# Kernel optimization log

Hardware: AMD Instinct MI355X
Metric: run time of the kernel (lower is better)

Reference implementation:

```python
import jax, jax.numpy as jnp
import numpy as np
from jax import lax

SCALES = [2 ** i for i in range(9)]  # h_grid_global(9, 2**8): dyadic scales 1..256
EPS = 2e-5


def conv1d(x, w, dil, pad):
    # x: [B, Cin, X], w: [Cout, Cin, k]; 'same'-style padding pad on each side, rhs dilation dil
    return lax.conv_general_dilated(x, w, window_strides=(1,), padding=[(pad, pad)],
                                    rhs_dilation=(dil,), dimension_numbers=('NCH', 'OIH', 'NCH'))


def maxpool2_x(x):
    # max pool kernel=2 stride=2 over last (spatial) axis, floor mode like torch
    L = x.shape[-1]
    L2 = (L // 2) * 2
    x = x[..., :L2]
    return jnp.max(x.reshape(x.shape[:-1] + (L2 // 2, 2)), axis=-1)


def lift_conv(x, w):
    k = w.shape[-1]
    outs = [conv1d(x, w, s, s * (k // 2)) / s for s in SCALES]
    return jnp.stack(outs, axis=2)


def gg_conv(x, w):
    # GConvGG with h_crop: x [B, Cin, H, X], w [Cout, Cin, nh=3, k] -> [B, Cout, H-2, X]
    # output scale index i uses input scale slabs i..i+2, x-dilation = scale_i, 1/scale_i normalization
    B, Cin, H, X = x.shape
    Cout, _, nh, k = w.shape
    wf = w.reshape(Cout, Cin * nh, k)
    outs = []
    for i in range(H - nh + 1):
        xi = x[:, :, i:i + nh, :].reshape(B, Cin * nh, X)
        s = SCALES[i]
        outs.append(conv1d(xi, wf, s, s * (k // 2)) / s)
    return jnp.stack(outs, axis=2)


def batchnorm(x, g, b):
    # BatchNorm2d (training batch stats, biased var) over [B, C, H, X]
    m = jnp.mean(x, axis=(0, 2, 3), keepdims=True)
    v = jnp.mean((x - m) ** 2, axis=(0, 2, 3), keepdims=True)
    gb = g[None, :, None, None]
    bb = b[None, :, None, None]
    return gb * (x - m) * lax.rsqrt(v + EPS) + bb


def _winit(key, shape):
    fan = int(np.prod(shape[1:]))
    return jax.random.normal(key, shape, dtype=jnp.float32) * (fan ** -0.5)


def setup_inputs() -> dict:
    key = jax.random.key(0)
    ks = jax.random.split(key, 12)
    B = 4096
    nc = 12
    x = jax.random.normal(ks[0], (B, 100, 6), dtype=jnp.float32)
    inp = {
        'x': x,
        'w1': _winit(ks[1], (nc, 6, 7)),
        'w2': _winit(ks[2], (nc * 2, nc, 3, 5)),
        'w3': _winit(ks[3], (nc * 4, nc * 2, 3, 5)),
        'w4': _winit(ks[4], (nc * 8, nc * 4, 3, 3)),
        'g1': jnp.ones((nc,), jnp.float32), 'b1': jnp.zeros((nc,), jnp.float32),
        'g2': jnp.ones((nc * 2,), jnp.float32), 'b2': jnp.zeros((nc * 2,), jnp.float32),
        'g3': jnp.ones((nc * 4,), jnp.float32), 'b3': jnp.zeros((nc * 4,), jnp.float32),
        'g4': jnp.ones((nc * 8,), jnp.float32), 'b4': jnp.zeros((nc * 8,), jnp.float32),
        'f1w': _winit(ks[5], (nc * 8, nc * 8 * 3)), 'f1b': jnp.zeros((nc * 8,), jnp.float32),
        'f2w': _winit(ks[6], (nc * 4, nc * 8)), 'f2b': jnp.zeros((nc * 4,), jnp.float32),
        'f3w': _winit(ks[7], (6, nc * 4)), 'f3b': jnp.zeros((6,), jnp.float32),
    }
    return inp


def reference(x, w1, w2, w3, w4, g1, b1, g2, b2, g3, b3, g4, b4,
              f1w, f1b, f2w, f2b, f3w, f3b):
    h = jnp.transpose(x, (0, 2, 1))          # [B, 6, 100]
    h = lift_conv(h, w1)                     # [B, 12, 9, 100]
    h = maxpool2_x(h)                        # [B, 12, 9, 50]
    h = batchnorm(jax.nn.relu(h), g1, b1)
    h = maxpool2_x(h)                        # [B, 12, 9, 25]
    h = gg_conv(h, w2)                       # [B, 24, 7, 25]
    h = maxpool2_x(h)                        # [B, 24, 7, 12]
    h = batchnorm(jax.nn.relu(h), g2, b2)
    h = maxpool2_x(h)                        # [B, 24, 7, 6]
    h = gg_conv(h, w3)                       # [B, 48, 5, 6]
    h = maxpool2_x(h)                        # [B, 48, 5, 3]
    h = batchnorm(jax.nn.relu(h), g3, b3)
    h = gg_conv(h, w4)                       # [B, 96, 3, 3]
    h = maxpool2_x(h)                        # [B, 96, 3, 1]
    h = batchnorm(jax.nn.relu(h), g4, b4)
    h = h.reshape(h.shape[0], -1)            # [B, 288]
    h = h @ f1w.T + f1b                      # dropout is identity in eval
    h = h @ f2w.T + f2b
    return h @ f3w.T + f3b                   # [B, 6]
```

## Files before the change

### kernel.cpp

```cpp
#include <hip/hip_runtime.h>
#include <hip/hip_fp16.h>

#define EPSBN 2e-5f

typedef _Float16 hf2 __attribute__((ext_vector_type(2)));

static __device__ __forceinline__ float fdot2h(hf2 a, hf2 b, float c) {
  return __builtin_amdgcn_fdot2(a, b, c, false);
}
static __device__ __forceinline__ unsigned pk(float a, float b) {
  union { __half2 h; unsigned u; } u;
  u.h = __floats2half2_rn(a, b);
  return u.u;
}

__global__ __launch_bounds__(256) void k_prep(const float* __restrict__ w1,
    const float* __restrict__ w2, const float* __restrict__ w3, const float* __restrict__ w4,
    __half* __restrict__ W1P, __half* __restrict__ W2P,
    __half* __restrict__ W3P, __half* __restrict__ W4P) {
  int i = blockIdx.x * 256 + threadIdx.x;
  if (i < 504) {
    int ci = i & 1, r = i >> 1, o = r % 12, j = (r / 12) % 7, cp = r / 84, c = 2 * cp + ci;
    W1P[i] = __float2half_rn(w1[(o * 6 + c) * 7 + j]);
  }
  if (i < 4320) {
    int ci = i & 1, r = i >> 1, o = r % 24, j = (r / 24) % 5, h = (r / 120) % 3, cp = r / 360;
    int c = 2 * cp + ci;
    W2P[i] = __float2half_rn(w2[((o * 12 + c) * 3 + h) * 5 + j]);
  }
  if (i < 17280) {
    int ci = i & 1, r = i >> 1, o = r % 48, j = (r / 48) % 5, h = (r / 240) % 3, cp = r / 720;
    int c = 2 * cp + ci;
    W3P[i] = __float2half_rn(w3[((o * 24 + c) * 3 + h) * 5 + j]);
  }
  if (i < 41472) {
    int ci = i & 1, r = i >> 1, o48 = r % 48, j = (r / 48) % 3, h = (r / 144) % 3;
    int cp = (r / 432) % 24, ch = r / 10368, c = 2 * cp + ci, o = ch * 48 + o48;
    W4P[i] = __float2half_rn(w4[((o * 48 + c) * 3 + h) * 3 + j]);
  }
}

#define NB1 4
template<int SI>
__device__ __forceinline__ void s1_si(const unsigned* __restrict__ xsu, int bb, int t0,
    const unsigned* __restrict__ wlu, int o0, bool act, int b,
    __half* __restrict__ r1, float& ts0, float& tq0, float& ts1, float& tq1) {
  constexpr int S = 1 << SI;
  float a0[10], a1[10];
#pragma unroll
  for (int k = 0; k < 10; ++k) { a0[k] = 0.f; a1[k] = 0.f; }
#pragma unroll 1
  for (int cp = 0; cp < 3; ++cp) {
    const hf2* xr = (const hf2*)xsu + (bb * 3 + cp) * 295 + 96 + t0;
    const unsigned* wp = wlu + cp * 84;
#pragma unroll
    for (int j = 0; j < 7; ++j) {
      const int off = S * (j - 3);
      if (off < -96 || off > 98) continue;
      hf2 w0 = *(const hf2*)(wp + j * 12 + o0);
      hf2 w1 = *(const hf2*)(wp + j * 12 + o0 + 1);
      hf2 xv[10];
#pragma unroll
      for (int k = 0; k < 10; ++k) xv[k] = xr[off + k];
#pragma unroll
      for (int k = 0; k < 10; ++k) {
        a0[k] = fdot2h(xv[k], w0, a0[k]);
        a1[k] = fdot2h(xv[k], w1, a1[k]);
      }
    }
  }
  if (act) {
    const float inv = 1.0f / (float)S;
    size_t rb = ((size_t)b * 12 + o0) * 9 + SI;
#pragma unroll
    for (int u = 0; u < 5; ++u) {
      float v0 = fmaxf(fmaxf(a0[2 * u], a0[2 * u + 1]) * inv, 0.f);
      float v1 = fmaxf(fmaxf(a1[2 * u], a1[2 * u + 1]) * inv, 0.f);
      r1[rb * 50 + (t0 >> 1) + u] = __float2half_rn(v0);
      r1[(rb + 9) * 50 + (t0 >> 1) + u] = __float2half_rn(v1);
      ts0 += v0; tq0 += v0 * v0; ts1 += v1; tq1 += v1 * v1;
    }
  }
}

__global__ __launch_bounds__(256) void k_lift(const float* __restrict__ x,
    const __half* __restrict__ W1P, __half* __restrict__ r1,
    float* __restrict__ sum, float* __restrict__ sq) {
  __shared__ unsigned xsu[NB1 * 885];
  __shared__ unsigned wlu[252];
  __shared__ float ssum[12], ssq[12];
  int b0 = blockIdx.x * NB1, tid = threadIdx.x;
  for (int i = tid; i < NB1 * 885; i += 256) xsu[i] = 0u;
  for (int i = tid; i < 252; i += 256) wlu[i] = ((const unsigned*)W1P)[i];
  if (tid < 12) { ssum[tid] = 0.f; ssq[tid] = 0.f; }
  __syncthreads();
  __half* xsh = (__half*)xsu;
  for (int i = tid; i < NB1 * 600; i += 256) {
    int bb = i / 600, f = i % 600, t = f / 6, c = f % 6;
    xsh[((bb * 3 + (c >> 1)) * 295 + 96 + t) * 2 + (c & 1)] =
        __float2half_rn(x[(size_t)(b0 + bb) * 600 + f]);
  }
  __syncthreads();
  bool act = tid < 240;
  int task = act ? tid : 0;
  int bb = task / 60, r = task % 60;
  int op = r / 10, tc = r % 10;
  int o0 = op * 2, t0 = tc * 10;
  int b = b0 + bb;
  float ts0 = 0.f, tq0 = 0.f, ts1 = 0.f, tq1 = 0.f;
  s1_si<0>(xsu, bb, t0, wlu, o0, act, b, r1, ts0, tq0, ts1, tq1);
  s1_si<1>(xsu, bb, t0, wlu, o0, act, b, r1, ts0, tq0, ts1, tq1);
  s1_si<2>(xsu, bb, t0, wlu, o0, act, b, r1, ts0, tq0, ts1, tq1);
  s1_si<3>(xsu, bb, t0, wlu, o0, act, b, r1, ts0, tq0, ts1, tq1);
  s1_si<4>(xsu, bb, t0, wlu, o0, act, b, r1, ts0, tq0, ts1, tq1);
  s1_si<5>(xsu, bb, t0, wlu, o0, act, b, r1, ts0, tq0, ts1, tq1);
  s1_si<6>(xsu, bb, t0, wlu, o0, act, b, r1, ts0, tq0, ts1, tq1);
  s1_si<7>(xsu, bb, t0, wlu, o0, act, b, r1, ts0, tq0, ts1, tq1);
  s1_si<8>(xsu, bb, t0, wlu, o0, act, b, r1, ts0, tq0, ts1, tq1);
  if (act) {
    atomicAdd(&ssum[o0], ts0); atomicAdd(&ssq[o0], tq0);
    atomicAdd(&ssum[o0 + 1], ts1); atomicAdd(&ssq[o0 + 1], tq1);
  }
  __syncthreads();
  if (tid < 12) { atomicAdd(&sum[tid], ssum[tid]); atomicAdd(&sq[tid], ssq[tid]); }
}

__global__ void k_bnstat(const float* __restrict__ sum, const float* __restrict__ sq,
    const float* __restrict__ g, const float* __restrict__ bb,
    float* __restrict__ sc, float* __restrict__ sh, int C, float invN) {
  int c = threadIdx.x;
  if (c < C) {
    float m = sum[c] * invN;
    float v = sq[c] * invN - m * m;
    float scale = g[c] * rsqrtf(v + EPSBN);
    sc[c] = scale;
    sh[c] = bb[c] - m * scale;
  }
}

#define NB2 5
template<int S, int I2>
__device__ __forceinline__ void s2_do(const unsigned* __restrict__ abu,
    const unsigned* __restrict__ wlu, int op, bool act, int b,
    __half* __restrict__ r2p, float& ts0, float& tq0, float& ts1, float& tq1) {
  float acc0[24], acc1[24];
#pragma unroll
  for (int t = 0; t < 24; ++t) { acc0[t] = 0.f; acc1[t] = 0.f; }
#pragma unroll 1
  for (int cp = 0; cp < 6; ++cp) {
#pragma unroll
    for (int h = 0; h < 3; ++h) {
      const hf2* ar = (const hf2*)(abu + (cp * 9 + I2 + h) * 26);
      hf2 rr[25];
#pragma unroll
      for (int t = 0; t < 25; ++t) rr[t] = ar[t];
      const unsigned* wp = wlu + ((cp * 3 + h) * 5) * 24 + op * 2;
#pragma unroll
      for (int j = 0; j < 5; ++j) {
        const int off = S * (j - 2);
        if (off <= -25 || off >= 25) continue;
        hf2 w0 = *(const hf2*)(wp + j * 24);
        hf2 w1 = *(const hf2*)(wp + j * 24 + 1);
#pragma unroll
        for (int t = 0; t < 24; ++t) {
          if (t + off >= 0 && t + off < 25) {
            acc0[t] = fdot2h(rr[t + off], w0, acc0[t]);
            acc1[t] = fdot2h(rr[t + off], w1, acc1[t]);
          }
        }
      }
    }
  }
  if (act) {
    const float inv = 1.0f / (float)S;
    int o0 = op * 2;
    __half* p0 = r2p + ((size_t)b * 24 + o0) * 42 + I2 * 6;
    __half* p1 = p0 + 42;
    float m0 = 0.f, m1 = 0.f;
#pragma unroll
    for (int u = 0; u < 12; ++u) {
      float v0 = fmaxf(fmaxf(acc0[2 * u], acc0[2 * u + 1]) * inv, 0.f);
      float v1 = fmaxf(fmaxf(acc1[2 * u], acc1[2 * u + 1]) * inv, 0.f);
      ts0 += v0; tq0 += v0 * v0; ts1 += v1; tq1 += v1 * v1;
      if ((u & 1) == 0) { m0 = v0; m1 = v1; }
      else {
        p0[u >> 1] = __float2half_rn(fmaxf(m0, v0));
        p1[u >> 1] = __float2half_rn(fmaxf(m1, v1));
      }
    }
  }
}

__global__ __launch_bounds__(256) void k_stage2(const __half* __restrict__ r1,
    const __half* __restrict__ W2P, const float* __restrict__ sc, const float* __restrict__ sh,
    __half* __restrict__ r2p, float* __restrict__ sum, float* __restrict__ sq, int B) {
  __shared__ unsigned asu[NB2 * 1405];
  __shared__ unsigned wlu[2160];
  __shared__ float ssum[24], ssq[24];
  int b0 = blockIdx.x * NB2, tid = threadIdx.x;
  for (int i = tid; i < NB2 * 1350; i += 256) {
    int bb = i / 1350, s = i % 1350;
    if (b0 + bb < B) {
      int cp = s / 225, rem = s % 225, row = rem / 25, t = rem % 25;
      int c0 = 2 * cp, c1 = c0 + 1;
      float2 a0 = __half22float2(*(const __half2*)(r1 +
          (((size_t)(b0 + bb) * 12 + c0) * 9 + row) * 50 + 2 * t));
      float2 a1 = __half22float2(*(const __half2*)(r1 +
          (((size_t)(b0 + bb) * 12 + c1) * 9 + row) * 50 + 2 * t));
      float v0 = fmaxf(a0.x, a0.y) * sc[c0] + sh[c0];
      float v1 = fmaxf(a1.x, a1.y) * sc[c1] + sh[c1];
      asu[bb * 1405 + (cp * 9 + row) * 26 + t] = pk(v0, v1);
    }
  }
  for (int i = tid; i < 540; i += 256)
    ((uint4*)wlu)[i] = ((const uint4*)W2P)[i];
  if (tid < 24) { ssum[tid] = 0.f; ssq[tid] = 0.f; }
  __syncthreads();
  int wv = tid >> 6, lane = tid & 63;
  int bb = lane / 12, op = lane % 12;
  bool act = (lane < 60) && (b0 + bb < B);
  if (bb > 4) bb = 4;
  const unsigned* abu = asu + bb * 1405;
  int b = b0 + bb;
  float ts0 = 0.f, tq0 = 0.f, ts1 = 0.f, tq1 = 0.f;
  if (wv == 0) {
    s2_do<1, 0>(abu, wlu, op, act, b, r2p, ts0, tq0, ts1, tq1);
  } else if (wv == 1) {
    s2_do<2, 1>(abu, wlu, op, act, b, r2p, ts0, tq0, ts1, tq1);
    s2_do<64, 6>(abu, wlu, op, act, b, r2p, ts0, tq0, ts1, tq1);
  } else if (wv == 2) {
    s2_do<4, 2>(abu, wlu, op, act, b, r2p, ts0, tq0, ts1, tq1);
    s2_do<32, 5>(abu, wlu, op, act, b, r2p, ts0, tq0, ts1, tq1);
  } else {
    s2_do<8, 3>(abu, wlu, op, act, b, r2p, ts0, tq0, ts1, tq1);
    s2_do<16, 4>(abu, wlu, op, act, b, r2p, ts0, tq0, ts1, tq1);
  }
  if (act) {
    int o0 = op * 2;
    atomicAdd(&ssum[o0], ts0); atomicAdd(&ssq[o0], tq0);
    atomicAdd(&ssum[o0 + 1], ts1); atomicAdd(&ssq[o0 + 1], tq1);
  }
  __syncthreads();
  if (tid < 24) { atomicAdd(&sum[tid], ssum[tid]); atomicAdd(&sq[tid], ssq[tid]); }
}

#define NB3 8
template<int I2>
__device__ __forceinline__ void s3h(const hf2* __restrict__ rr, int h,
    const hf2* __restrict__ w0, const hf2* __restrict__ w1, float* __restrict__ acc) {
  constexpr int S = 1 << I2;
  const int base = (I2 + h) * 6;
#pragma unroll
  for (int j = 0; j < 5; ++j) {
    const int off = S * (j - 2);
    if (off <= -6 || off >= 6) continue;
#pragma unroll
    for (int t = 0; t < 6; ++t) {
      if (t + off >= 0 && t + off < 6) {
        acc[t] = fdot2h(rr[base + t + off], w0[j], acc[t]);
        acc[6 + t] = fdot2h(rr[base + t + off], w1[j], acc[6 + t]);
      }
    }
  }
}

__global__ __launch_bounds__(256) void k_stage3(const __half* __restrict__ r2p,
    const __half* __restrict__ W3P, const float* __restrict__ sc, const float* __restrict__ sh,
    __half* __restrict__ r3, float* __restrict__ sum, float* __restrict__ sq) {
  __shared__ unsigned asu[NB3 * 505];
  __shared__ unsigned wlu[8640];
  __shared__ float ssum[48], ssq[48];
  int b0 = blockIdx.x * NB3, tid = threadIdx.x;
  for (int i = tid; i < NB3 * 252; i += 256) {
    int bb = i / 252, s = i % 252;
    int cp = s / 21, rem = s % 21, row = rem / 3, tp = rem % 3;
    int c0 = 2 * cp, c1 = c0 + 1;
    float2 a0 = __half22float2(*(const __half2*)(r2p +
        (((size_t)(b0 + bb) * 24 + c0) * 7 + row) * 6 + 2 * tp));
    float2 a1 = __half22float2(*(const __half2*)(r2p +
        (((size_t)(b0 + bb) * 24 + c1) * 7 + row) * 6 + 2 * tp));
    float v00 = a0.x * sc[c0] + sh[c0], v01 = a0.y * sc[c0] + sh[c0];
    float v10 = a1.x * sc[c1] + sh[c1], v11 = a1.y * sc[c1] + sh[c1];
    int di = bb * 505 + (cp * 7 + row) * 6 + 2 * tp;
    asu[di] = pk(v00, v10);
    asu[di + 1] = pk(v01, v11);
  }
  for (int i = tid; i < 2160; i += 256)
    ((uint4*)wlu)[i] = ((const uint4*)W3P)[i];
  if (tid < 48) { ssum[tid] = 0.f; ssq[tid] = 0.f; }
  __syncthreads();
  bool act = tid < 192;
  int bb = act ? tid / 24 : 0, op = tid % 24;
  int b = b0 + bb;
  if (act) {
    float acc[60];
#pragma unroll
    for (int k = 0; k < 60; ++k) acc[k] = 0.f;
#pragma unroll 1
    for (int cp = 0; cp < 12; ++cp) {
      const hf2* ar = (const hf2*)(asu + bb * 505 + cp * 42);
      hf2 rr[42];
#pragma unroll
      for (int k = 0; k < 42; ++k) rr[k] = ar[k];
#pragma unroll
      for (int h = 0; h < 3; ++h) {
        const unsigned* wp = wlu + (cp * 15 + h * 5) * 48 + op * 2;
        hf2 w0[5], w1[5];
#pragma unroll
        for (int j = 0; j < 5; ++j) {
          w0[j] = *(const hf2*)(wp + j * 48);
          w1[j] = *(const hf2*)(wp + j * 48 + 1);
        }
        s3h<0>(rr, h, w0, w1, acc);
        s3h<1>(rr, h, w0, w1, acc + 12);
        s3h<2>(rr, h, w0, w1, acc + 24);
        s3h<3>(rr, h, w0, w1, acc + 36);
        s3h<4>(rr, h, w0, w1, acc + 48);
      }
    }
    float ts0 = 0.f, tq0 = 0.f, ts1 = 0.f, tq1 = 0.f;
    int ob = op * 2;
#pragma unroll
    for (int i2 = 0; i2 < 5; ++i2) {
      const float inv = 1.0f / (float)(1 << i2);
      size_t rb0 = ((size_t)b * 48 + ob) * 15 + i2 * 3;
#pragma unroll
      for (int u = 0; u < 3; ++u) {
        float v0 = fmaxf(fmaxf(acc[i2 * 12 + 2 * u], acc[i2 * 12 + 2 * u + 1]) * inv, 0.f);
        float v1 = fmaxf(fmaxf(acc[i2 * 12 + 6 + 2 * u], acc[i2 * 12 + 7 + 2 * u]) * inv, 0.f);
        r3[rb0 + u] = __float2half_rn(v0);
        r3[rb0 + 15 + u] = __float2half_rn(v1);
        ts0 += v0; tq0 += v0 * v0; ts1 += v1; tq1 += v1 * v1;
      }
    }
    atomicAdd(&ssum[ob], ts0); atomicAdd(&ssq[ob], tq0);
    atomicAdd(&ssum[ob + 1], ts1); atomicAdd(&ssq[ob + 1], tq1);
  }
  __syncthreads();
  if (tid < 48) { atomicAdd(&sum[tid], ssum[tid]); atomicAdd(&sq[tid], ssq[tid]); }
}

#define NB4 8
template<int I2>
__device__ __forceinline__ void s4h(const hf2* __restrict__ rr, int h,
    const hf2* __restrict__ w0, const hf2* __restrict__ w1, float* __restrict__ acc) {
  constexpr int S = 1 << I2;
  const int base = (I2 + h) * 3;
#pragma unroll
  for (int j = 0; j < 3; ++j) {
    const int off = S * (j - 1);
    if (off <= -3 || off >= 3) continue;
    if (off >= 0) {
      acc[0] = fdot2h(rr[base + off], w0[j], acc[0]);
      acc[2] = fdot2h(rr[base + off], w1[j], acc[2]);
    }
    const int i1 = 1 + off;
    if (i1 >= 0 && i1 < 3) {
      acc[1] = fdot2h(rr[base + i1], w0[j], acc[1]);
      acc[3] = fdot2h(rr[base + i1], w1[j], acc[3]);
    }
  }
}

__global__ __launch_bounds__(256) void k_stage4(const __half* __restrict__ r3,
    const __half* __restrict__ W4P, const float* __restrict__ sc, const float* __restrict__ sh,
    float* __restrict__ r4, float* __restrict__ sum, float* __restrict__ sq) {
  __shared__ unsigned asu[NB4 * 361];
  __shared__ unsigned wlu[10368];
  __shared__ float ssum[96], ssq[96];
  int b0 = blockIdx.x * NB4, tid = threadIdx.x;
  for (int i = tid; i < NB4 * 360; i += 256) {
    int bb = i / 360, s = i % 360;
    int cp = s / 15, rem = s % 15, row = rem / 3, t = rem % 3;
    int c0 = 2 * cp, c1 = c0 + 1;
    float v0 = __half2float(r3[(((size_t)(b0 + bb) * 48 + c0) * 5 + row) * 3 + t]) * sc[c0] + sh[c0];
    float v1 = __half2float(r3[(((size_t)(b0 + bb) * 48 + c1) * 5 + row) * 3 + t]) * sc[c1] + sh[c1];
    asu[bb * 361 + (cp * 5 + row) * 3 + t] = pk(v0, v1);
  }
  if (tid < 96) { ssum[tid] = 0.f; ssq[tid] = 0.f; }
  bool act = tid < 192;
  int bb = act ? tid / 24 : 0, op = tid % 24;
  int b = b0 + bb;
  for (int chunk = 0; chunk < 2; ++chunk) {
    __syncthreads();
    for (int i = tid; i < 2592; i += 256)
      ((uint4*)wlu)[i] = ((const uint4*)W4P)[chunk * 2592 + i];
    __syncthreads();
    if (act) {
      float acc[12];
#pragma unroll
      for (int k = 0; k < 12; ++k) acc[k] = 0.f;
#pragma unroll 1
      for (int cp = 0; cp < 24; ++cp) {
        const hf2* ar = (const hf2*)(asu + bb * 361 + cp * 15);
        hf2 rr[15];
#pragma unroll
        for (int k = 0; k < 15; ++k) rr[k] = ar[k];
#pragma unroll
        for (int h = 0; h < 3; ++h) {
          const unsigned* wp = wlu + ((cp * 3 + h) * 3) * 48 + op * 2;
          hf2 w0[3], w1[3];
#pragma unroll
          for (int j = 0; j < 3; ++j) {
            w0[j] = *(const hf2*)(wp + j * 48);
            w1[j] = *(const hf2*)(wp + j * 48 + 1);
          }
          s4h<0>(rr, h, w0, w1, acc);
          s4h<1>(rr, h, w0, w1, acc + 4);
          s4h<2>(rr, h, w0, w1, acc + 8);
        }
      }
      int o0 = chunk * 48 + op * 2;
#pragma unroll
      for (int oo = 0; oo < 2; ++oo) {
        float ts = 0.f, tq = 0.f;
#pragma unroll
        for (int i2 = 0; i2 < 3; ++i2) {
          const float inv = 1.0f / (float)(1 << i2);
          float v = fmaxf(fmaxf(acc[i2 * 4 + oo * 2], acc[i2 * 4 + oo * 2 + 1]) * inv, 0.f);
          r4[(size_t)b * 288 + (o0 + oo) * 3 + i2] = v;
          ts += v; tq += v * v;
        }
        atomicAdd(&ssum[o0 + oo], ts); atomicAdd(&ssq[o0 + oo], tq);
      }
    }
  }
  __syncthreads();
  if (tid < 96) { atomicAdd(&sum[tid], ssum[tid]); atomicAdd(&sq[tid], ssq[tid]); }
}

__global__ __launch_bounds__(256) void k_fc(const float* __restrict__ r4,
    const float* __restrict__ sc, const float* __restrict__ sh,
    const float* __restrict__ f1w, const float* __restrict__ f1b,
    const float* __restrict__ f2w, const float* __restrict__ f2b,
    const float* __restrict__ f3w, const float* __restrict__ f3b,
    float* __restrict__ out) {
  __shared__ float v[4][288];
  __shared__ float h1[4][96];
  __shared__ float h2[4][48];
  int b0 = blockIdx.x * 4, tid = threadIdx.x;
  for (int i = tid; i < 4 * 288; i += 256) {
    int bb = i / 288, f = i % 288, c = f / 3;
    v[bb][f] = r4[(size_t)(b0 + bb) * 288 + f] * sc[c] + sh[c];
  }
  __syncthreads();
  for (int d = tid; d < 384; d += 256) {
    int o = d >> 2, bb = d & 3;
    const float* wr = &f1w[o * 288];
    const float* vv = v[bb];
    float acc = f1b[o];
    for (int f = 0; f < 288; ++f) acc += wr[f] * vv[f];
    h1[bb][o] = acc;
  }
  __syncthreads();
  if (tid < 192) {
    int o = tid >> 2, bb = tid & 3;
    const float* wr = &f2w[o * 96];
    float acc = f2b[o];
    for (int f = 0; f < 96; ++f) acc += wr[f] * h1[bb][f];
    h2[bb][o] = acc;
  }
  __syncthreads();
  if (tid < 24) {
    int o = tid >> 2, bb = tid & 3;
    const float* wr = &f3w[o * 48];
    float acc = f3b[o];
    for (int f = 0; f < 48; ++f) acc += wr[f] * h2[bb][f];
    out[(size_t)(b0 + bb) * 6 + o] = acc;
  }
}

extern "C" void kernel_launch(void* const* d_in, const int* in_sizes, int n_in,
                              void* d_out, int out_size, void* d_ws, size_t ws_size,
                              hipStream_t stream) {
  const float* x   = (const float*)d_in[0];
  const float* w1  = (const float*)d_in[1];
  const float* w2  = (const float*)d_in[2];
  const float* w3  = (const float*)d_in[3];
  const float* w4  = (const float*)d_in[4];
  const float* g1  = (const float*)d_in[5];
  const float* b1  = (const float*)d_in[6];
  const float* g2  = (const float*)d_in[7];
  const float* b2  = (const float*)d_in[8];
  const float* g3  = (const float*)d_in[9];
  const float* b3  = (const float*)d_in[10];
  const float* g4  = (const float*)d_in[11];
  const float* b4  = (const float*)d_in[12];
  const float* f1w = (const float*)d_in[13];
  const float* f1b = (const float*)d_in[14];
  const float* f2w = (const float*)d_in[15];
  const float* f2b = (const float*)d_in[16];
  const float* f3w = (const float*)d_in[17];
  const float* f3b = (const float*)d_in[18];
  float* out = (float*)d_out;
  float* ws = (float*)d_ws;

  const int B = 4096;
  float* SUM1 = ws + 0;   float* SQ1 = ws + 12;
  float* SUM2 = ws + 24;  float* SQ2 = ws + 48;
  float* SUM3 = ws + 72;  float* SQ3 = ws + 120;
  float* SUM4 = ws + 168; float* SQ4 = ws + 264;
  float* SC1 = ws + 384;  float* SH1 = ws + 396;
  float* SC2 = ws + 408;  float* SH2 = ws + 432;
  float* SC3 = ws + 456;  float* SH3 = ws + 504;
  float* SC4 = ws + 552;  float* SH4 = ws + 648;
  __half* H0  = (__half*)(ws + 1024);
  __half* W1P = H0;
  __half* W2P = H0 + 512;
  __half* W3P = H0 + 4864;
  __half* W4P = H0 + 22272;
  __half* R1h = H0 + 65536;
  __half* R2p = R1h + (size_t)B * 5400;
  __half* R3h = R1h;
  float*  R4  = (float*)(R2p + (size_t)B * 1008);

  hipMemsetAsync(d_ws, 0, 384 * sizeof(float), stream);

  k_prep<<<162, 256, 0, stream>>>(w1, w2, w3, w4, W1P, W2P, W3P, W4P);
  k_lift<<<B / NB1, 256, 0, stream>>>(x, W1P, R1h, SUM1, SQ1);
  k_bnstat<<<1, 128, 0, stream>>>(SUM1, SQ1, g1, b1, SC1, SH1, 12, 1.0f / (float)(B * 450));
  k_stage2<<<(B + NB2 - 1) / NB2, 256, 0, stream>>>(R1h, W2P, SC1, SH1, R2p, SUM2, SQ2, B);
  k_bnstat<<<1, 128, 0, stream>>>(SUM2, SQ2, g2, b2, SC2, SH2, 24, 1.0f / (float)(B * 84));
  k_stage3<<<B / NB3, 256, 0, stream>>>(R2p, W3P, SC2, SH2, R3h, SUM3, SQ3);
  k_bnstat<<<1, 128, 0, stream>>>(SUM3, SQ3, g3, b3, SC3, SH3, 48, 1.0f / (float)(B * 15));
  k_stage4<<<B / NB4, 256, 0, stream>>>(R3h, W4P, SC3, SH3, R4, SUM4, SQ4);
  k_bnstat<<<1, 128, 0, stream>>>(SUM4, SQ4, g4, b4, SC4, SH4, 96, 1.0f / (float)(B * 3));
  k_fc<<<B / 4, 256, 0, stream>>>(R4, SC4, SH4, f1w, f1b, f2w, f2b, f3w, f3b, out);
}
```

Before: 321.3 us.

## Fold weight prep and BN stat kernels into stage kernels; pack intermediates as half2

Removes the separate weight-packing kernel by doing the weight conversion inside k_lift, and removes the four single-block BN-statistics kernels by computing scale and shift in each consumer kernel's prologue. Intermediates r2 and r3 are now stored channel-pair-interleaved as packed half2 words, so the next stage loads one 32-bit word per pair and no longer gathers two scattered halves. This cuts five launches and some strided traffic, at the cost of redundant per-block BN math and extra work in the first blocks of k_lift.

```diff
diff --git a/kernel.cpp b/kernel.cpp
--- a/kernel.cpp
+++ b/kernel.cpp
@@ -13,31 +13,9 @@
   u.h = __floats2half2_rn(a, b);
   return u.u;
 }
-
-__global__ __launch_bounds__(256) void k_prep(const float* __restrict__ w1,
-    const float* __restrict__ w2, const float* __restrict__ w3, const float* __restrict__ w4,
-    __half* __restrict__ W1P, __half* __restrict__ W2P,
-    __half* __restrict__ W3P, __half* __restrict__ W4P) {
-  int i = blockIdx.x * 256 + threadIdx.x;
-  if (i < 504) {
-    int ci = i & 1, r = i >> 1, o = r % 12, j = (r / 12) % 7, cp = r / 84, c = 2 * cp + ci;
-    W1P[i] = __float2half_rn(w1[(o * 6 + c) * 7 + j]);
-  }
-  if (i < 4320) {
-    int ci = i & 1, r = i >> 1, o = r % 24, j = (r / 24) % 5, h = (r / 120) % 3, cp = r / 360;
-    int c = 2 * cp + ci;
-    W2P[i] = __float2half_rn(w2[((o * 12 + c) * 3 + h) * 5 + j]);
-  }
-  if (i < 17280) {
-    int ci = i & 1, r = i >> 1, o = r % 48, j = (r / 48) % 5, h = (r / 240) % 3, cp = r / 720;
-    int c = 2 * cp + ci;
-    W3P[i] = __float2half_rn(w3[((o * 24 + c) * 3 + h) * 5 + j]);
-  }
-  if (i < 41472) {
-    int ci = i & 1, r = i >> 1, o48 = r % 48, j = (r / 48) % 3, h = (r / 144) % 3;
-    int cp = (r / 432) % 24, ch = r / 10368, c = 2 * cp + ci, o = ch * 48 + o48;
-    W4P[i] = __float2half_rn(w4[((o * 48 + c) * 3 + h) * 3 + j]);
-  }
+static __device__ __forceinline__ float2 uph(unsigned v) {
+  union { unsigned u; __half2 h; } x; x.u = v;
+  return __half22float2(x.h);
 }
 
 #define NB1 4
@@ -84,14 +62,37 @@
 }
 
 __global__ __launch_bounds__(256) void k_lift(const float* __restrict__ x,
-    const __half* __restrict__ W1P, __half* __restrict__ r1,
-    float* __restrict__ sum, float* __restrict__ sq) {
-  __shared__ unsigned xsu[NB1 * 885];
-  __shared__ unsigned wlu[252];
+    const float* __restrict__ w1, const float* __restrict__ w2,
+    const float* __restrict__ w3, const float* __restrict__ w4,
+    __half* __restrict__ W2P, __half* __restrict__ W3P, __half* __restrict__ W4P,
+    __half* __restrict__ r1, float* __restrict__ sum, float* __restrict__ sq) {
+  __shared__ __align__(16) unsigned xsu[NB1 * 885];
+  __shared__ __align__(16) unsigned wlu[252];
   __shared__ float ssum[12], ssq[12];
   int b0 = blockIdx.x * NB1, tid = threadIdx.x;
+  {
+    int gi = blockIdx.x * 256 + tid;
+    if (gi < 4320) {
+      int ci = gi & 1, r = gi >> 1, o = r % 24, j = (r / 24) % 5, h = (r / 120) % 3, cp = r / 360;
+      int c = 2 * cp + ci;
+      W2P[gi] = __float2half_rn(w2[((o * 12 + c) * 3 + h) * 5 + j]);
+    } else if (gi < 21600) {
+      int k = gi - 4320;
+      int ci = k & 1, r = k >> 1, o = r % 48, j = (r / 48) % 5, h = (r / 240) % 3, cp = r / 720;
+      int c = 2 * cp + ci;
+      W3P[k] = __float2half_rn(w3[((o * 24 + c) * 3 + h) * 5 + j]);
+    } else if (gi < 63072) {
+      int k = gi - 21600;
+      int ci = k & 1, r = k >> 1, o48 = r % 48, j = (r / 48) % 3, h = (r / 144) % 3;
+      int cp = (r / 432) % 24, ch = r / 10368, c = 2 * cp + ci, o = ch * 48 + o48;
+      W4P[k] = __float2half_rn(w4[((o * 48 + c) * 3 + h) * 3 + j]);
+    }
+  }
   for (int i = tid; i < NB1 * 885; i += 256) xsu[i] = 0u;
-  for (int i = tid; i < 252; i += 256) wlu[i] = ((const unsigned*)W1P)[i];
+  for (int i = tid; i < 252; i += 256) {
+    int cp = i / 84, j = (i % 84) / 12, o = i % 12;
+    wlu[i] = pk(w1[(o * 6 + 2 * cp) * 7 + j], w1[(o * 6 + 2 * cp + 1) * 7 + j]);
+  }
   if (tid < 12) { ssum[tid] = 0.f; ssq[tid] = 0.f; }
   __syncthreads();
   __half* xsh = (__half*)xsu;
@@ -125,24 +126,11 @@
   if (tid < 12) { atomicAdd(&sum[tid], ssum[tid]); atomicAdd(&sq[tid], ssq[tid]); }
 }
 
-__global__ void k_bnstat(const float* __restrict__ sum, const float* __restrict__ sq,
-    const float* __restrict__ g, const float* __restrict__ bb,
-    float* __restrict__ sc, float* __restrict__ sh, int C, float invN) {
-  int c = threadIdx.x;
-  if (c < C) {
-    float m = sum[c] * invN;
-    float v = sq[c] * invN - m * m;
-    float scale = g[c] * rsqrtf(v + EPSBN);
-    sc[c] = scale;
-    sh[c] = bb[c] - m * scale;
-  }
-}
-
 #define NB2 5
 template<int S, int I2>
 __device__ __forceinline__ void s2_do(const unsigned* __restrict__ abu,
     const unsigned* __restrict__ wlu, int op, bool act, int b,
-    __half* __restrict__ r2p, float& ts0, float& tq0, float& ts1, float& tq1) {
+    unsigned* __restrict__ r2p, float& ts0, float& tq0, float& ts1, float& tq1) {
   float acc0[24], acc1[24];
 #pragma unroll
   for (int t = 0; t < 24; ++t) { acc0[t] = 0.f; acc1[t] = 0.f; }
@@ -173,9 +161,7 @@
   }
   if (act) {
     const float inv = 1.0f / (float)S;
-    int o0 = op * 2;
-    __half* p0 = r2p + ((size_t)b * 24 + o0) * 42 + I2 * 6;
-    __half* p1 = p0 + 42;
+    unsigned* pd = r2p + ((size_t)b * 12 + op) * 42 + I2 * 6;
     float m0 = 0.f, m1 = 0.f;
 #pragma unroll
     for (int u = 0; u < 12; ++u) {
@@ -183,21 +169,30 @@
       float v1 = fmaxf(fmaxf(acc1[2 * u], acc1[2 * u + 1]) * inv, 0.f);
       ts0 += v0; tq0 += v0 * v0; ts1 += v1; tq1 += v1 * v1;
       if ((u & 1) == 0) { m0 = v0; m1 = v1; }
-      else {
-        p0[u >> 1] = __float2half_rn(fmaxf(m0, v0));
-        p1[u >> 1] = __float2half_rn(fmaxf(m1, v1));
-      }
+      else pd[u >> 1] = pk(fmaxf(m0, v0), fmaxf(m1, v1));
     }
   }
 }
 
 __global__ __launch_bounds__(256) void k_stage2(const __half* __restrict__ r1,
-    const __half* __restrict__ W2P, const float* __restrict__ sc, const float* __restrict__ sh,
-    __half* __restrict__ r2p, float* __restrict__ sum, float* __restrict__ sq, int B) {
-  __shared__ unsigned asu[NB2 * 1405];
-  __shared__ unsigned wlu[2160];
+    const __half* __restrict__ W2P,
+    const float* __restrict__ SUM, const float* __restrict__ SQ,
+    const float* __restrict__ g, const float* __restrict__ bbn, float invN,
+    unsigned* __restrict__ r2p, float* __restrict__ sum, float* __restrict__ sq, int B) {
+  __shared__ __align__(16) unsigned asu[NB2 * 1405];
+  __shared__ __align__(16) unsigned wlu[2160];
   __shared__ float ssum[24], ssq[24];
+  __shared__ float scf[12], shf[12];
   int b0 = blockIdx.x * NB2, tid = threadIdx.x;
+  if (tid < 12) {
+    float m = SUM[tid] * invN;
+    float v = SQ[tid] * invN - m * m;
+    float scale = g[tid] * rsqrtf(v + EPSBN);
+    scf[tid] = scale; shf[tid] = bbn[tid] - m * scale;
+    ssum[tid] = 0.f; ssq[tid] = 0.f;
+    ssum[tid + 12] = 0.f; ssq[tid + 12] = 0.f;
+  }
+  __syncthreads();
   for (int i = tid; i < NB2 * 1350; i += 256) {
     int bb = i / 1350, s = i % 1350;
     if (b0 + bb < B) {
@@ -207,14 +202,13 @@
           (((size_t)(b0 + bb) * 12 + c0) * 9 + row) * 50 + 2 * t));
       float2 a1 = __half22float2(*(const __half2*)(r1 +
           (((size_t)(b0 + bb) * 12 + c1) * 9 + row) * 50 + 2 * t));
-      float v0 = fmaxf(a0.x, a0.y) * sc[c0] + sh[c0];
-      float v1 = fmaxf(a1.x, a1.y) * sc[c1] + sh[c1];
+      float v0 = fmaxf(a0.x, a0.y) * scf[c0] + shf[c0];
+      float v1 = fmaxf(a1.x, a1.y) * scf[c1] + shf[c1];
       asu[bb * 1405 + (cp * 9 + row) * 26 + t] = pk(v0, v1);
     }
   }
   for (int i = tid; i < 540; i += 256)
     ((uint4*)wlu)[i] = ((const uint4*)W2P)[i];
-  if (tid < 24) { ssum[tid] = 0.f; ssq[tid] = 0.f; }
   __syncthreads();
   int wv = tid >> 6, lane = tid & 63;
   int bb = lane / 12, op = lane % 12;
@@ -264,30 +258,32 @@
   }
 }
 
-__global__ __launch_bounds__(256) void k_stage3(const __half* __restrict__ r2p,
-    const __half* __restrict__ W3P, const float* __restrict__ sc, const float* __restrict__ sh,
-    __half* __restrict__ r3, float* __restrict__ sum, float* __restrict__ sq) {
-  __shared__ unsigned asu[NB3 * 505];
-  __shared__ unsigned wlu[8640];
+__global__ __launch_bounds__(256) void k_stage3(const unsigned* __restrict__ r2p,
+    const __half* __restrict__ W3P,
+    const float* __restrict__ SUM, const float* __restrict__ SQ,
+    const float* __restrict__ g, const float* __restrict__ bbn, float invN,
+    unsigned* __restrict__ r3, float* __restrict__ sum, float* __restrict__ sq) {
+  __shared__ __align__(16) unsigned asu[NB3 * 505];
+  __shared__ __align__(16) unsigned wlu[8640];
   __shared__ float ssum[48], ssq[48];
+  __shared__ float scf[24], shf[24];
   int b0 = blockIdx.x * NB3, tid = threadIdx.x;
-  for (int i = tid; i < NB3 * 252; i += 256) {
-    int bb = i / 252, s = i % 252;
-    int cp = s / 21, rem = s % 21, row = rem / 3, tp = rem % 3;
+  if (tid < 24) {
+    float m = SUM[tid] * invN;
+    float v = SQ[tid] * invN - m * m;
+    float scale = g[tid] * rsqrtf(v + EPSBN);
+    scf[tid] = scale; shf[tid] = bbn[tid] - m * scale;
+  }
+  if (tid < 48) { ssum[tid] = 0.f; ssq[tid] = 0.f; }
+  __syncthreads();
+  for (int i = tid; i < NB3 * 504; i += 256) {
+    int bb = i / 504, f = i % 504, cp = f / 42;
     int c0 = 2 * cp, c1 = c0 + 1;
-    float2 a0 = __half22float2(*(const __half2*)(r2p +
-        (((size_t)(b0 + bb) * 24 + c0) * 7 + row) * 6 + 2 * tp));
-    float2 a1 = __half22float2(*(const __half2*)(r2p +
-        (((size_t)(b0 + bb) * 24 + c1) * 7 + row) * 6 + 2 * tp));
-    float v00 = a0.x * sc[c0] + sh[c0], v01 = a0.y * sc[c0] + sh[c0];
-    float v10 = a1.x * sc[c1] + sh[c1], v11 = a1.y * sc[c1] + sh[c1];
-    int di = bb * 505 + (cp * 7 + row) * 6 + 2 * tp;
-    asu[di] = pk(v00, v10);
-    asu[di + 1] = pk(v01, v11);
+    float2 a = uph(r2p[(size_t)(b0 + bb) * 504 + f]);
+    asu[bb * 505 + f] = pk(a.x * scf[c0] + shf[c0], a.y * scf[c1] + shf[c1]);
   }
   for (int i = tid; i < 2160; i += 256)
     ((uint4*)wlu)[i] = ((const uint4*)W3P)[i];
-  if (tid < 48) { ssum[tid] = 0.f; ssq[tid] = 0.f; }
   __syncthreads();
   bool act = tid < 192;
   int bb = act ? tid / 24 : 0, op = tid % 24;
@@ -323,13 +319,12 @@
 #pragma unroll
     for (int i2 = 0; i2 < 5; ++i2) {
       const float inv = 1.0f / (float)(1 << i2);
-      size_t rb0 = ((size_t)b * 48 + ob) * 15 + i2 * 3;
+      size_t rb = ((size_t)b * 24 + op) * 15 + i2 * 3;
 #pragma unroll
       for (int u = 0; u < 3; ++u) {
         float v0 = fmaxf(fmaxf(acc[i2 * 12 + 2 * u], acc[i2 * 12 + 2 * u + 1]) * inv, 0.f);
         float v1 = fmaxf(fmaxf(acc[i2 * 12 + 6 + 2 * u], acc[i2 * 12 + 7 + 2 * u]) * inv, 0.f);
-        r3[rb0 + u] = __float2half_rn(v0);
-        r3[rb0 + 15 + u] = __float2half_rn(v1);
+        r3[rb + u] = pk(v0, v1);
         ts0 += v0; tq0 += v0 * v0; ts1 += v1; tq1 += v1 * v1;
       }
     }
@@ -362,22 +357,30 @@
   }
 }
 
-__global__ __launch_bounds__(256) void k_stage4(const __half* __restrict__ r3,
-    const __half* __restrict__ W4P, const float* __restrict__ sc, const float* __restrict__ sh,
+__global__ __launch_bounds__(256) void k_stage4(const unsigned* __restrict__ r3,
+    const __half* __restrict__ W4P,
+    const float* __restrict__ SUM, const float* __restrict__ SQ,
+    const float* __restrict__ g, const float* __restrict__ bbn, float invN,
     float* __restrict__ r4, float* __restrict__ sum, float* __restrict__ sq) {
-  __shared__ unsigned asu[NB4 * 361];
-  __shared__ unsigned wlu[10368];
+  __shared__ __align__(16) unsigned asu[NB4 * 361];
+  __shared__ __align__(16) unsigned wlu[10368];
   __shared__ float ssum[96], ssq[96];
+  __shared__ float scf[48], shf[48];
   int b0 = blockIdx.x * NB4, tid = threadIdx.x;
+  if (tid < 48) {
+    float m = SUM[tid] * invN;
+    float v = SQ[tid] * invN - m * m;
+    float scale = g[tid] * rsqrtf(v + EPSBN);
+    scf[tid] = scale; shf[tid] = bbn[tid] - m * scale;
+  }
+  if (tid < 96) { ssum[tid] = 0.f; ssq[tid] = 0.f; }
+  __syncthreads();
   for (int i = tid; i < NB4 * 360; i += 256) {
-    int bb = i / 360, s = i % 360;
-    int cp = s / 15, rem = s % 15, row = rem / 3, t = rem % 3;
+    int bb = i / 360, f = i % 360, cp = f / 15;
     int c0 = 2 * cp, c1 = c0 + 1;
-    float v0 = __half2float(r3[(((size_t)(b0 + bb) * 48 + c0) * 5 + row) * 3 + t]) * sc[c0] + sh[c0];
-    float v1 = __half2float(r3[(((size_t)(b0 + bb) * 48 + c1) * 5 + row) * 3 + t]) * sc[c1] + sh[c1];
-    asu[bb * 361 + (cp * 5 + row) * 3 + t] = pk(v0, v1);
-  }
-  if (tid < 96) { ssum[tid] = 0.f; ssq[tid] = 0.f; }
+    float2 a = uph(r3[(size_t)(b0 + bb) * 360 + f]);
+    asu[bb * 361 + f] = pk(a.x * scf[c0] + shf[c0], a.y * scf[c1] + shf[c1]);
+  }
   bool act = tid < 192;
   int bb = act ? tid / 24 : 0, op = tid % 24;
   int b = b0 + bb;
@@ -430,7 +433,8 @@
 }
 
 __global__ __launch_bounds__(256) void k_fc(const float* __restrict__ r4,
-    const float* __restrict__ sc, const float* __restrict__ sh,
+    const float* __restrict__ SUM, const float* __restrict__ SQ,
+    const float* __restrict__ g, const float* __restrict__ bbn, float invN,
     const float* __restrict__ f1w, const float* __restrict__ f1b,
     const float* __restrict__ f2w, const float* __restrict__ f2b,
     const float* __restrict__ f3w, const float* __restrict__ f3b,
@@ -438,10 +442,18 @@
   __shared__ float v[4][288];
   __shared__ float h1[4][96];
   __shared__ float h2[4][48];
+  __shared__ float scf[96], shf[96];
   int b0 = blockIdx.x * 4, tid = threadIdx.x;
+  if (tid < 96) {
+    float m = SUM[tid] * invN;
+    float vv = SQ[tid] * invN - m * m;
+    float scale = g[tid] * rsqrtf(vv + EPSBN);
+    scf[tid] = scale; shf[tid] = bbn[tid] - m * scale;
+  }
+  __syncthreads();
   for (int i = tid; i < 4 * 288; i += 256) {
     int bb = i / 288, f = i % 288, c = f / 3;
-    v[bb][f] = r4[(size_t)(b0 + bb) * 288 + f] * sc[c] + sh[c];
+    v[bb][f] = r4[(size_t)(b0 + bb) * 288 + f] * scf[c] + shf[c];
   }
   __syncthreads();
   for (int d = tid; d < 384; d += 256) {
@@ -500,30 +512,24 @@
   float* SUM2 = ws + 24;  float* SQ2 = ws + 48;
   float* SUM3 = ws + 72;  float* SQ3 = ws + 120;
   float* SUM4 = ws + 168; float* SQ4 = ws + 264;
-  float* SC1 = ws + 384;  float* SH1 = ws + 396;
-  float* SC2 = ws + 408;  float* SH2 = ws + 432;
-  float* SC3 = ws + 456;  float* SH3 = ws + 504;
-  float* SC4 = ws + 552;  float* SH4 = ws + 648;
   __half* H0  = (__half*)(ws + 1024);
-  __half* W1P = H0;
-  __half* W2P = H0 + 512;
-  __half* W3P = H0 + 4864;
-  __half* W4P = H0 + 22272;
+  __half* W2P = H0;
+  __half* W3P = H0 + 4320;
+  __half* W4P = H0 + 21600;
   __half* R1h = H0 + 65536;
-  __half* R2p = R1h + (size_t)B * 5400;
-  __half* R3h = R1h;
-  float*  R4  = (float*)(R2p + (size_t)B * 1008);
+  unsigned* R2P = (unsigned*)(R1h + (size_t)B * 5400);
+  unsigned* R3D = (unsigned*)R1h;
+  float*  R4  = (float*)(R2P + (size_t)B * 504);
 
   hipMemsetAsync(d_ws, 0, 384 * sizeof(float), stream);
 
-  k_prep<<<162, 256, 0, stream>>>(w1, w2, w3, w4, W1P, W2P, W3P, W4P);
-  k_lift<<<B / NB1, 256, 0, stream>>>(x, W1P, R1h, SUM1, SQ1);
-  k_bnstat<<<1, 128, 0, stream>>>(SUM1, SQ1, g1, b1, SC1, SH1, 12, 1.0f / (float)(B * 450));
-  k_stage2<<<(B + NB2 - 1) / NB2, 256, 0, stream>>>(R1h, W2P, SC1, SH1, R2p, SUM2, SQ2, B);
-  k_bnstat<<<1, 128, 0, stream>>>(SUM2, SQ2, g2, b2, SC2, SH2, 24, 1.0f / (float)(B * 84));
-  k_stage3<<<B / NB3, 256, 0, stream>>>(R2p, W3P, SC2, SH2, R3h, SUM3, SQ3);
-  k_bnstat<<<1, 128, 0, stream>>>(SUM3, SQ3, g3, b3, SC3, SH3, 48, 1.0f / (float)(B * 15));
-  k_stage4<<<B / NB4, 256, 0, stream>>>(R3h, W4P, SC3, SH3, R4, SUM4, SQ4);
-  k_bnstat<<<1, 128, 0, stream>>>(SUM4, SQ4, g4, b4, SC4, SH4, 96, 1.0f / (float)(B * 3));
-  k_fc<<<B / 4, 256, 0, stream>>>(R4, SC4, SH4, f1w, f1b, f2w, f2b, f3w, f3b, out);
-}
+  k_lift<<<B / NB1, 256, 0, stream>>>(x, w1, w2, w3, w4, W2P, W3P, W4P, R1h, SUM1, SQ1);
+  k_stage2<<<(B + NB2 - 1) / NB2, 256, 0, stream>>>(R1h, W2P, SUM1, SQ1, g1, b1,
+      1.0f / (float)(B * 450), R2P, SUM2, SQ2, B);
+  k_stage3<<<B / NB3, 256, 0, stream>>>(R2P, W3P, SUM2, SQ2, g2, b2,
+      1.0f / (float)(B * 84), R3D, SUM3, SQ3);
+  k_stage4<<<B / NB4, 256, 0, stream>>>(R3D, W4P, SUM3, SQ3, g3, b3,
+      1.0f / (float)(B * 15), R4, SUM4, SQ4);
+  k_fc<<<B / 4, 256, 0, stream>>>(R4, SUM4, SQ4, g4, b4,
+      1.0f / (float)(B * 3), f1w, f1b, f2w, f2b, f3w, f3b, out);
+}
```

New measurement: 299.5 us. 1.07x faster.
